# Performance work log

Measured on AMD Instinct MI355X. Metric: run time of the kernel, lower is better.

## Reference

```python
import jax, jax.numpy as jnp
import numpy as np

HEADS = 4
A_DIMS = 64
V_DIMS = 64
NODES_NUM = 128
F_DIMS = 256
LN_EPS = 1e-5


def setup_inputs() -> dict:
    key = jax.random.key(0)
    ks = jax.random.split(key, 7)
    b, n = 8, 8192
    x = jax.random.normal(ks[0], (b, n, F_DIMS), dtype=jnp.float32)
    nodes = jax.random.normal(ks[1], (NODES_NUM, A_DIMS), dtype=jnp.float32)
    Wa = jax.random.normal(ks[2], (F_DIMS, A_DIMS * HEADS), dtype=jnp.float32) * (F_DIMS ** -0.5)
    Wv = jax.random.normal(ks[3], (F_DIMS, V_DIMS * HEADS), dtype=jnp.float32) * (F_DIMS ** -0.5)
    bv = jax.random.normal(ks[4], (V_DIMS * HEADS,), dtype=jnp.float32) * 0.02
    gamma = jnp.ones((V_DIMS * HEADS,), dtype=jnp.float32)
    beta = jnp.zeros((V_DIMS * HEADS,), dtype=jnp.float32)
    return {"x": x, "nodes": nodes, "Wa": Wa, "Wv": Wv, "bv": bv, "gamma": gamma, "beta": beta}


def reference(x, nodes, Wa, Wv, bv, gamma, beta):
    b, n, d = x.shape
    scale = A_DIMS ** -0.5
    # projections: (b, n, h*d) -> (b, h, n, d)
    a = (x @ Wa).reshape(b, n, HEADS, A_DIMS).transpose(0, 2, 1, 3)
    v = (x @ Wv + bv).reshape(b, n, HEADS, V_DIMS).transpose(0, 2, 1, 3)
    # learned-query cross attention: nodes shared across heads
    attn = jnp.einsum('id,bhjd->bhij', nodes, a) * scale  # (b, h, nodes, n)
    attn = jax.nn.softmax(attn, axis=-1)
    out = jnp.einsum('bhij,bhjd->bhid', attn, v)  # (b, h, nodes, v)
    out = out.transpose(0, 2, 1, 3).reshape(b, NODES_NUM, HEADS * V_DIMS)
    out = jnp.where(out >= 0, out, 0.2 * out)  # leaky_relu(0.2)
    mu = jnp.mean(out, axis=-1, keepdims=True)
    var = jnp.mean((out - mu) ** 2, axis=-1, keepdims=True)
    out = (out - mu) * jax.lax.rsqrt(var + LN_EPS) * gamma + beta
    return out
```

## Files before the change

### kernel.cpp

```cpp
#include <hip/hip_runtime.h>
#include <math.h>

typedef float f32x4 __attribute__((ext_vector_type(4)));
typedef short s16x8 __attribute__((ext_vector_type(8)));
typedef unsigned short u16;
typedef u16 u16x4 __attribute__((ext_vector_type(4)));
typedef unsigned int u32;

#define NCH 16
#define NT  16

__device__ __forceinline__ u16 f2bf(float f){
  union { float f; u32 u; } v; v.f = f;
  u32 r = v.u + 0x7FFFu + ((v.u >> 16) & 1u);
  return (u16)(r >> 16);
}
__device__ __forceinline__ float bf2f(u16 b){
  union { u32 u; float f; } v; v.u = ((u32)b) << 16; return v.f;
}
__device__ __forceinline__ f32x4 mfma16(s16x8 a, s16x8 b, f32x4 c){
  return __builtin_amdgcn_mfma_f32_16x16x32_bf16(a, b, c, 0, 0, 0);
}

__global__ __launch_bounds__(256) void k0_cvt(const float* __restrict__ x,
                                              u16* __restrict__ xbf, u16* __restrict__ xT){
  __shared__ u16 T[64*68];
  const int tid = threadIdx.x;
  const int bx = blockIdx.x;
  const int b = bx >> 9, rest = bx & 511, jt = rest >> 2, ft = rest & 3;
  const float* xp = x + (long)b*2097152 + (long)jt*16384 + ft*64;
  u16* xbp = xbf + (long)b*2097152 + (long)jt*16384 + ft*64;
  #pragma unroll
  for (int p=0;p<4;++p){
    int e = p*1024 + tid*4;
    int row = e >> 6, f = e & 63;
    float4 v = *(const float4*)(xp + (long)row*256 + f);
    u16x4 u = { f2bf(v.x), f2bf(v.y), f2bf(v.z), f2bf(v.w) };
    *(u16x4*)(xbp + (long)row*256 + f) = u;
    *(u16x4*)&T[row*68 + f] = u;
  }
  __syncthreads();
  u16* xtp = xT + (long)b*2097152 + (long)(ft*64)*8192 + (long)jt*64;
  #pragma unroll
  for (int p=0;p<4;++p){
    int e = p*1024 + tid*4;
    int fr = e >> 6, j = e & 63;
    u16x4 u = { T[j*68 + fr], T[(j+1)*68 + fr], T[(j+2)*68 + fr], T[(j+3)*68 + fr] };
    *(u16x4*)(xtp + (long)fr*8192 + j) = u;
  }
}

__global__ __launch_bounds__(256) void k1_q(const float* __restrict__ nodes,
    const float* __restrict__ Wa, u16* __restrict__ Qbf){
  __shared__ float nd[64];
  const int bx = blockIdx.x;
  const int h = bx >> 7, i = bx & 127;
  const int tid = threadIdx.x;
  if (tid < 64) nd[tid] = nodes[i*64 + tid];
  __syncthreads();
  const float* wp = Wa + tid*256 + h*64;
  float acc = 0.f;
  #pragma unroll
  for (int d=0; d<64; d+=4){
    float4 wv = *(const float4*)(wp + d);
    acc += nd[d]*wv.x + nd[d+1]*wv.y + nd[d+2]*wv.z + nd[d+3]*wv.w;
  }
  Qbf[(h*128 + i)*256 + tid] = f2bf(acc * 0.125f);
}

__global__ __launch_bounds__(256,2) void k2_attn(const u16* __restrict__ xbf,
    const u16* __restrict__ xT, const u16* __restrict__ Qbf,
    u16* __restrict__ ctxp, float* __restrict__ stats){
  __shared__ u16 Xs[32*264];
  __shared__ u16 XTs[256*40];
  __shared__ u16 Pl[64*40];
  __shared__ float flds[64];

  const int tid = threadIdx.x;
  const int l = tid & 63, w = tid >> 6;
  const int li = l & 15, g = l >> 4;
  const int nbL = w * 16;

  const int idx = blockIdx.x;
  const int q  = idx & 127;
  const int hh = idx >> 7;
  const int h = hh & 3, half = hh >> 2;
  const int b = q >> 4, ch = q & 15;
  const int nodeG = half*64 + nbL;

  s16x8 qf[8];
  #pragma unroll
  for (int kf=0; kf<8; ++kf)
    qf[kf] = *(const s16x8*)(Qbf + ((h*128 + nodeG + li)*256 + kf*32 + g*8));

  f32x4 cacc[16];
  #pragma unroll
  for (int ff=0;ff<16;++ff){ f32x4 z = {0.f,0.f,0.f,0.f}; cacc[ff] = z; }

  float m0 = -INFINITY, ls0 = 0.f;

  const u16* xb  = xbf + (long)b*2097152 + (long)ch*131072;
  const u16* xtb = xT  + (long)b*2097152 + (long)ch*512;

  s16x8 pXs[4], pXT[4];
  #pragma unroll
  for (int p=0;p<4;++p){
    pXs[p] = *(const s16x8*)(xb + (long)(p*8 + (tid>>5))*256 + (tid&31)*8);
    pXT[p] = *(const s16x8*)(xtb + (long)(p*64 + (tid>>2))*8192 + (tid&3)*8);
  }

  for (int tt=0; tt<NT; ++tt){
    __syncthreads();
    #pragma unroll
    for (int p=0;p<4;++p){
      *(s16x8*)&Xs[(p*8 + (tid>>5))*264 + (tid&31)*8] = pXs[p];
      *(s16x8*)&XTs[(p*64 + (tid>>2))*40 + (tid&3)*8] = pXT[p];
    }
    if (tt+1 < NT){
      const long jb = (long)(tt+1)*32;
      #pragma unroll
      for (int p=0;p<4;++p){
        pXs[p] = *(const s16x8*)(xb + (jb + p*8 + (tid>>5))*256 + (tid&31)*8);
        pXT[p] = *(const s16x8*)(xtb + (long)(p*64 + (tid>>2))*8192 + jb + (tid&3)*8);
      }
    }
    __syncthreads();

    f32x4 s00={0.f,0.f,0.f,0.f}, s10={0.f,0.f,0.f,0.f};
    #pragma unroll
    for (int kf=0; kf<8; ++kf){
      s16x8 ax0 = *(const s16x8*)&Xs[li*264 + kf*32 + g*8];
      s16x8 ax1 = *(const s16x8*)&Xs[(16+li)*264 + kf*32 + g*8];
      s00 = mfma16(ax0, qf[kf], s00);
      s10 = mfma16(ax1, qf[kf], s10);
    }

    float t0 = fmaxf(fmaxf(fmaxf(s00[0],s00[1]),fmaxf(s00[2],s00[3])),
                     fmaxf(fmaxf(s10[0],s10[1]),fmaxf(s10[2],s10[3])));
    t0 = fmaxf(t0, __shfl_xor(t0,16)); t0 = fmaxf(t0, __shfl_xor(t0,32));
    float mn0 = fmaxf(m0,t0);
    float fac0 = __expf(m0-mn0);
    #pragma unroll
    for (int rr=0;rr<4;++rr){
      s00[rr]=__expf(s00[rr]-mn0); s10[rr]=__expf(s10[rr]-mn0);
    }
    float u0 = s00[0]+s00[1]+s00[2]+s00[3] + s10[0]+s10[1]+s10[2]+s10[3];
    u0 += __shfl_xor(u0,16); u0 += __shfl_xor(u0,32);
    ls0 = ls0*fac0 + u0;
    const bool nochange = __all(fac0==1.0f);
    m0 = mn0;

    {
      u16x4 p00 = { f2bf(s00[0]),f2bf(s00[1]),f2bf(s00[2]),f2bf(s00[3]) };
      u16x4 p10 = { f2bf(s10[0]),f2bf(s10[1]),f2bf(s10[2]),f2bf(s10[3]) };
      *(u16x4*)&Pl[(nbL+li)*40 + g*4]      = p00;
      *(u16x4*)&Pl[(nbL+li)*40 + 16 + g*4] = p10;
    }
    if (g==0){ flds[nbL+li] = fac0; }

    if (!nochange){
      float fr0[4];
      #pragma unroll
      for (int rr=0;rr<4;++rr){ fr0[rr] = flds[nbL + g*4 + rr]; }
      #pragma unroll
      for (int ff=0; ff<16; ++ff)
        #pragma unroll
        for (int rr=0;rr<4;++rr){ cacc[ff][rr]*=fr0[rr]; }
    }

    s16x8 pa0 = *(const s16x8*)&Pl[(nbL+li)*40 + g*8];
    #pragma unroll
    for (int ff=0; ff<16; ++ff){
      s16x8 bx = *(const s16x8*)&XTs[(ff*16+li)*40 + g*8];
      cacc[ff] = mfma16(pa0, bx, cacc[ff]);
    }
  }

  const int sb = ((b*4 + h)*NCH + ch)*128;
  if (g==0){
    stats[2*(sb + nodeG + li)    ] = m0;
    stats[2*(sb + nodeG + li) + 1] = ls0;
  }
  u16* cp = ctxp + (long)sb*256;
  #pragma unroll
  for (int ff=0;ff<16;++ff)
    #pragma unroll
    for (int rr=0;rr<4;++rr){
      int node = nodeG + g*4 + rr;
      int f = ff*16 + li;
      cp[(long)node*256 + f] = f2bf(cacc[ff][rr]);
    }
}

__global__ __launch_bounds__(256) void k3_out(const u16* __restrict__ ctxp,
    const float* __restrict__ stats, const float* __restrict__ Wv,
    const float* __restrict__ bv, const float* __restrict__ gamma,
    const float* __restrict__ beta, float* __restrict__ out){
  __shared__ float ctxL[4*256];
  __shared__ float red[8];
  const int tid = threadIdx.x;
  const int bx = blockIdx.x;
  const int b = bx >> 7, node = bx & 127;
  #pragma unroll
  for (int h=0; h<4; ++h){
    float mc[NCH], lc[NCH];
    #pragma unroll
    for (int c=0;c<NCH;++c){
      int si = ((b*4+h)*NCH + c)*128 + node;
      mc[c] = stats[2*si]; lc[c] = stats[2*si+1];
    }
    float mm = mc[0];
    #pragma unroll
    for (int c=1;c<NCH;++c) mm = fmaxf(mm, mc[c]);
    float L = 0.f, acc = 0.f;
    #pragma unroll
    for (int c=0;c<NCH;++c){
      float wc = __expf(mc[c]-mm);
      L += wc*lc[c];
      acc += wc * bf2f(ctxp[((long)((b*4+h)*NCH + c)*128 + node)*256 + tid]);
    }
    ctxL[h*256 + tid] = acc / L;
  }
  __syncthreads();
  const int hh = tid >> 6;
  float o = bv[tid];
  const float* cx = &ctxL[hh*256];
  #pragma unroll 8
  for (int f=0; f<256; ++f) o = fmaf(cx[f], Wv[f*256 + tid], o);
  o = (o >= 0.f) ? o : 0.2f*o;
  float s1 = o, s2 = o*o;
  #pragma unroll
  for (int d=1; d<64; d<<=1){ s1 += __shfl_xor(s1,d); s2 += __shfl_xor(s2,d); }
  if ((tid&63)==0){ red[tid>>6] = s1; red[4 + (tid>>6)] = s2; }
  __syncthreads();
  float S1 = red[0]+red[1]+red[2]+red[3];
  float S2 = red[4]+red[5]+red[6]+red[7];
  float mu = S1 * (1.f/256.f);
  float var = S2 * (1.f/256.f) - mu*mu;
  float rs = rsqrtf(fmaxf(var, 0.f) + 1e-5f);
  out[(long)(b*128 + node)*256 + tid] = (o - mu)*rs*gamma[tid] + beta[tid];
}

extern "C" void kernel_launch(void* const* d_in, const int* in_sizes, int n_in,
                              void* d_out, int out_size, void* d_ws, size_t ws_size,
                              hipStream_t stream){
  const float* x     = (const float*)d_in[0];
  const float* nodes = (const float*)d_in[1];
  const float* Wa    = (const float*)d_in[2];
  const float* Wv    = (const float*)d_in[3];
  const float* bv    = (const float*)d_in[4];
  const float* gamma = (const float*)d_in[5];
  const float* beta  = (const float*)d_in[6];
  float* out = (float*)d_out;

  u16* xbf  = (u16*)d_ws;
  u16* xT   = xbf + 16777216;
  u16* Qbf  = xT + 16777216;
  u16* ctxp = Qbf + 131072;
  float* stats = (float*)(ctxp + 16777216);

  k0_cvt<<<dim3(4096), dim3(256), 0, stream>>>(x, xbf, xT);
  k1_q  <<<dim3(512),  dim3(256), 0, stream>>>(nodes, Wa, Qbf);
  k2_attn<<<dim3(1024), dim3(256), 0, stream>>>(xbf, xT, Qbf, ctxp, stats);
  k3_out<<<dim3(1024), dim3(256), 0, stream>>>(ctxp, stats, Wv, bv, gamma, beta, out);
}
```

Measured before the change: 115.7 us.

## Stream X tiles into double-buffered LDS via direct global_load_lds with swizzle

Replaces the register-staged load of the X tile with direct global-to-LDS async loads (global_load_lds), double-buffered across iterations and using an XOR swizzle instead of padding to avoid bank conflicts. Manual s_waitcnt/s_barrier sequences replace the __syncthreads pairs so the next tile's load overlaps current compute. It also drops the occupancy hint of 2 blocks per CU in launch_bounds, which frees registers but may reduce occupancy. Hand-written vmcnt counts are fragile; if they miscount the outstanding loads, the code reads stale data.

```diff
diff --git a/kernel.cpp b/kernel.cpp
--- a/kernel.cpp
+++ b/kernel.cpp
@@ -20,6 +20,10 @@
 }
 __device__ __forceinline__ f32x4 mfma16(s16x8 a, s16x8 b, f32x4 c){
   return __builtin_amdgcn_mfma_f32_16x16x32_bf16(a, b, c, 0, 0, 0);
+}
+__device__ __forceinline__ void gload16(const void* g, void* l){
+  __builtin_amdgcn_global_load_lds((const __attribute__((address_space(1))) void*)g,
+                                   (__attribute__((address_space(3))) void*)l, 16, 0, 0);
 }
 
 __global__ __launch_bounds__(256) void k0_cvt(const float* __restrict__ x,
@@ -68,10 +72,10 @@
   Qbf[(h*128 + i)*256 + tid] = f2bf(acc * 0.125f);
 }
 
-__global__ __launch_bounds__(256,2) void k2_attn(const u16* __restrict__ xbf,
+__global__ __launch_bounds__(256) void k2_attn(const u16* __restrict__ xbf,
     const u16* __restrict__ xT, const u16* __restrict__ Qbf,
     u16* __restrict__ ctxp, float* __restrict__ stats){
-  __shared__ u16 Xs[32*264];
+  __shared__ u16 Xs2[2][32*256];
   __shared__ u16 XTs[256*40];
   __shared__ u16 Pl[64*40];
   __shared__ float flds[64];
@@ -102,35 +106,50 @@
   const u16* xb  = xbf + (long)b*2097152 + (long)ch*131072;
   const u16* xtb = xT  + (long)b*2097152 + (long)ch*512;
 
-  s16x8 pXs[4], pXT[4];
-  #pragma unroll
-  for (int p=0;p<4;++p){
-    pXs[p] = *(const s16x8*)(xb + (long)(p*8 + (tid>>5))*256 + (tid&31)*8);
+  s16x8 pXT[4];
+  #pragma unroll
+  for (int p=0;p<4;++p)
     pXT[p] = *(const s16x8*)(xtb + (long)(p*64 + (tid>>2))*8192 + (tid&3)*8);
-  }
-
+  __builtin_amdgcn_sched_barrier(0);
+  #pragma unroll
+  for (int c=0;c<4;++c){
+    int j = w*8 + c*2 + (l>>5);
+    int unit = (l & 31) ^ (j & 7);
+    gload16(xb + (size_t)j*256 + unit*8, &Xs2[0][(size_t)(w*4+c)*512]);
+  }
+
+  int cur = 0;
   for (int tt=0; tt<NT; ++tt){
-    __syncthreads();
-    #pragma unroll
-    for (int p=0;p<4;++p){
-      *(s16x8*)&Xs[(p*8 + (tid>>5))*264 + (tid&31)*8] = pXs[p];
+    asm volatile("s_waitcnt lgkmcnt(0)\n\ts_barrier" ::: "memory");
+
+    #pragma unroll
+    for (int p=0;p<4;++p)
       *(s16x8*)&XTs[(p*64 + (tid>>2))*40 + (tid&3)*8] = pXT[p];
-    }
     if (tt+1 < NT){
-      const long jb = (long)(tt+1)*32;
-      #pragma unroll
-      for (int p=0;p<4;++p){
-        pXs[p] = *(const s16x8*)(xb + (jb + p*8 + (tid>>5))*256 + (tid&31)*8);
+      const int jb = (tt+1)*32;
+      #pragma unroll
+      for (int p=0;p<4;++p)
         pXT[p] = *(const s16x8*)(xtb + (long)(p*64 + (tid>>2))*8192 + jb + (tid&3)*8);
+      __builtin_amdgcn_sched_barrier(0);
+      #pragma unroll
+      for (int c=0;c<4;++c){
+        int j = w*8 + c*2 + (l>>5);
+        int unit = (l & 31) ^ (j & 7);
+        gload16(xb + (size_t)(jb + j)*256 + unit*8, &Xs2[cur^1][(size_t)(w*4+c)*512]);
       }
-    }
-    __syncthreads();
+      asm volatile("s_waitcnt vmcnt(8) lgkmcnt(0)\n\ts_barrier" ::: "memory");
+    } else {
+      asm volatile("s_waitcnt vmcnt(0) lgkmcnt(0)\n\ts_barrier" ::: "memory");
+    }
+
+    const u16* Xc = &Xs2[cur][0];
 
     f32x4 s00={0.f,0.f,0.f,0.f}, s10={0.f,0.f,0.f,0.f};
     #pragma unroll
     for (int kf=0; kf<8; ++kf){
-      s16x8 ax0 = *(const s16x8*)&Xs[li*264 + kf*32 + g*8];
-      s16x8 ax1 = *(const s16x8*)&Xs[(16+li)*264 + kf*32 + g*8];
+      int u0 = ((kf*4+g) ^ (li&7))*8;
+      s16x8 ax0 = *(const s16x8*)&Xc[ li*256 + u0];
+      s16x8 ax1 = *(const s16x8*)&Xc[(16+li)*256 + u0];
       s00 = mfma16(ax0, qf[kf], s00);
       s10 = mfma16(ax1, qf[kf], s10);
     }
@@ -144,9 +163,9 @@
     for (int rr=0;rr<4;++rr){
       s00[rr]=__expf(s00[rr]-mn0); s10[rr]=__expf(s10[rr]-mn0);
     }
-    float u0 = s00[0]+s00[1]+s00[2]+s00[3] + s10[0]+s10[1]+s10[2]+s10[3];
-    u0 += __shfl_xor(u0,16); u0 += __shfl_xor(u0,32);
-    ls0 = ls0*fac0 + u0;
+    float u0s = s00[0]+s00[1]+s00[2]+s00[3] + s10[0]+s10[1]+s10[2]+s10[3];
+    u0s += __shfl_xor(u0s,16); u0s += __shfl_xor(u0s,32);
+    ls0 = ls0*fac0 + u0s;
     const bool nochange = __all(fac0==1.0f);
     m0 = mn0;
 
@@ -174,6 +193,7 @@
       s16x8 bx = *(const s16x8*)&XTs[(ff*16+li)*40 + g*8];
       cacc[ff] = mfma16(pa0, bx, cacc[ff]);
     }
+    cur ^= 1;
   }
 
   const int sb = ((b*4 + h)*NCH + ch)*128;
```

Result: slower. 124.9 us (+7.9%).

## Read X and X-transpose tiles directly from global memory instead of LDS staging

Applied to the files above, without the earlier changes.

The attention kernel stops staging the X and transposed-X tiles through shared memory with register prefetch and two block barriers per iteration. Each wave now loads its MFMA operands straight from global memory, relying on the L1/L2 caches for reuse across the four waves. The launch-bounds occupancy hint is also dropped. This removes LDS traffic and the barriers, but each wave now issues redundant, less coalesced global loads (the transposed loads are strided by 8192 elements) and has no explicit prefetch to hide latency.

```diff
diff --git a/kernel.cpp b/kernel.cpp
--- a/kernel.cpp
+++ b/kernel.cpp
@@ -68,11 +68,9 @@
   Qbf[(h*128 + i)*256 + tid] = f2bf(acc * 0.125f);
 }
 
-__global__ __launch_bounds__(256,2) void k2_attn(const u16* __restrict__ xbf,
+__global__ __launch_bounds__(256) void k2_attn(const u16* __restrict__ xbf,
     const u16* __restrict__ xT, const u16* __restrict__ Qbf,
     u16* __restrict__ ctxp, float* __restrict__ stats){
-  __shared__ u16 Xs[32*264];
-  __shared__ u16 XTs[256*40];
   __shared__ u16 Pl[64*40];
   __shared__ float flds[64];
 
@@ -102,35 +100,14 @@
   const u16* xb  = xbf + (long)b*2097152 + (long)ch*131072;
   const u16* xtb = xT  + (long)b*2097152 + (long)ch*512;
 
-  s16x8 pXs[4], pXT[4];
-  #pragma unroll
-  for (int p=0;p<4;++p){
-    pXs[p] = *(const s16x8*)(xb + (long)(p*8 + (tid>>5))*256 + (tid&31)*8);
-    pXT[p] = *(const s16x8*)(xtb + (long)(p*64 + (tid>>2))*8192 + (tid&3)*8);
-  }
-
   for (int tt=0; tt<NT; ++tt){
-    __syncthreads();
-    #pragma unroll
-    for (int p=0;p<4;++p){
-      *(s16x8*)&Xs[(p*8 + (tid>>5))*264 + (tid&31)*8] = pXs[p];
-      *(s16x8*)&XTs[(p*64 + (tid>>2))*40 + (tid&3)*8] = pXT[p];
-    }
-    if (tt+1 < NT){
-      const long jb = (long)(tt+1)*32;
-      #pragma unroll
-      for (int p=0;p<4;++p){
-        pXs[p] = *(const s16x8*)(xb + (jb + p*8 + (tid>>5))*256 + (tid&31)*8);
-        pXT[p] = *(const s16x8*)(xtb + (long)(p*64 + (tid>>2))*8192 + jb + (tid&3)*8);
-      }
-    }
-    __syncthreads();
+    const u16* xrow = xb + (long)tt*8192;
 
     f32x4 s00={0.f,0.f,0.f,0.f}, s10={0.f,0.f,0.f,0.f};
     #pragma unroll
     for (int kf=0; kf<8; ++kf){
-      s16x8 ax0 = *(const s16x8*)&Xs[li*264 + kf*32 + g*8];
-      s16x8 ax1 = *(const s16x8*)&Xs[(16+li)*264 + kf*32 + g*8];
+      s16x8 ax0 = *(const s16x8*)(xrow + (long)li*256 + kf*32 + g*8);
+      s16x8 ax1 = *(const s16x8*)(xrow + (long)(16+li)*256 + kf*32 + g*8);
       s00 = mfma16(ax0, qf[kf], s00);
       s10 = mfma16(ax1, qf[kf], s10);
     }
@@ -169,9 +146,10 @@
     }
 
     s16x8 pa0 = *(const s16x8*)&Pl[(nbL+li)*40 + g*8];
+    const u16* xtc = xtb + tt*32;
     #pragma unroll
     for (int ff=0; ff<16; ++ff){
-      s16x8 bx = *(const s16x8*)&XTs[(ff*16+li)*40 + g*8];
+      s16x8 bx = *(const s16x8*)(xtc + (long)(ff*16+li)*8192 + g*8);
       cacc[ff] = mfma16(pa0, bx, cacc[ff]);
     }
   }
```

After: 281.7 us. +143.4%, slower.
